# Performance work log

Measured on AMD Instinct MI355X. Metric: run time of the kernel, lower is better.

Reference implementation:

```python
import jax, jax.numpy as jnp
import numpy as np
import math

B, S, D_IN, D, H, L, NC = 4, 2048, 64, 512, 8, 2, 2
DK = D // H
FACTOR = 5
TOPK = min(FACTOR * int(math.log(S)), S)  # 35
EPS = 1e-5


def make_pe():
    # sinusoidal positional encoding [S, D]
    pos = jnp.arange(S, dtype=jnp.float32)[:, None]
    div = jnp.exp(jnp.arange(0, D, 2, dtype=jnp.float32) * (-math.log(10000.0) / D))
    pe = jnp.zeros((S, D), jnp.float32)
    pe = pe.at[:, 0::2].set(jnp.sin(pos * div)).at[:, 1::2].set(jnp.cos(pos * div))
    return pe


def layernorm(x, g, b):
    m = x.mean(-1, keepdims=True)
    v = x.var(-1, keepdims=True)
    return (x - m) / jnp.sqrt(v + EPS) * g + b


def setup_inputs() -> dict:
    key = jax.random.key(0)
    ks = iter(jax.random.split(key, 16))
    def p(shape, s=0.02):
        return jax.random.normal(next(ks), shape, jnp.float32) * s
    return dict(
        x=jax.random.normal(next(ks), (B, S, D_IN), jnp.float32),
        emb_w=p((D_IN, D)), emb_b=jnp.zeros((D,), jnp.float32),
        wq=p((L, D, D)), bq=jnp.zeros((L, D), jnp.float32),
        wk=p((L, D, D)), bk=jnp.zeros((L, D), jnp.float32),
        wv=p((L, D, D)), bv=jnp.zeros((L, D), jnp.float32),
        wo=p((L, D, D)), bo=jnp.zeros((L, D), jnp.float32),
        ff1_w=p((L, D, 4 * D)), ff1_b=jnp.zeros((L, 4 * D), jnp.float32),
        ff2_w=p((L, 4 * D, D)), ff2_b=jnp.zeros((L, D), jnp.float32),
        ln1_g=jnp.ones((L, D), jnp.float32), ln1_b=jnp.zeros((L, D), jnp.float32),
        ln2_g=jnp.ones((L, D), jnp.float32), ln2_b=jnp.zeros((L, D), jnp.float32),
        dec1_w=p((D, D // 2)), dec1_b=jnp.zeros((D // 2,), jnp.float32),
        dec2_w=p((D // 2, NC)), dec2_b=jnp.zeros((NC,), jnp.float32),
    )


def reference(x, emb_w, emb_b, wq, bq, wk, bk, wv, bv, wo, bo,
              ff1_w, ff1_b, ff2_w, ff2_b, ln1_g, ln1_b, ln2_g, ln2_b,
              dec1_w, dec1_b, dec2_w, dec2_b):
    h = x @ emb_w + emb_b + make_pe()[None]  # [B,S,D]
    scale = 1.0 / math.sqrt(DK)
    for i in range(L):
        q = (h @ wq[i] + bq[i]).reshape(B, S, H, DK).transpose(0, 2, 1, 3)
        k = (h @ wk[i] + bk[i]).reshape(B, S, H, DK).transpose(0, 2, 1, 3)
        v = (h @ wv[i] + bv[i]).reshape(B, S, H, DK).transpose(0, 2, 1, 3)
        scores = jnp.einsum('bhqd,bhkd->bhqk', q, k) * scale  # [B,H,S,S]
        top_scores, _ = jax.lax.top_k(scores, TOPK)            # [B,H,S,TOPK]
        attn = jax.nn.softmax(top_scores, axis=-1)
        # NOTE: faithful to source quirk — V sliced to its FIRST TOPK rows,
        # top_indices are discarded by the original module.
        ao = jnp.einsum('bhqk,bhkd->bhqd', attn, v[:, :, :TOPK, :])
        ao = ao.transpose(0, 2, 1, 3).reshape(B, S, D) @ wo[i] + bo[i]
        h = layernorm(h + ao, ln1_g[i], ln1_b[i])
        ff = jax.nn.relu(h @ ff1_w[i] + ff1_b[i]) @ ff2_w[i] + ff2_b[i]
        h = layernorm(h + ff, ln2_g[i], ln2_b[i])
    pooled = h.mean(axis=1)  # AdaptiveAvgPool1d(1) over seq
    out = jax.nn.relu(pooled @ dec1_w + dec1_b) @ dec2_w + dec2_b  # [B,NC]
    return out
```

## Files before the change

kernel.cpp:

```cpp
#include <hip/hip_runtime.h>
#include <cmath>

typedef unsigned short u16;
typedef __attribute__((ext_vector_type(8))) short short8;
typedef __attribute__((ext_vector_type(4))) float float4v;
typedef unsigned short ushort2v __attribute__((ext_vector_type(2)));

#define S_LEN 2048
#define NTOK  8192
#define TOPK  35
#define NT512 ((size_t)NTOK*512)

__device__ __forceinline__ u16 f2b(float f){
  unsigned int x = __float_as_uint(f);
  unsigned int r = (x + 0x7fffu + ((x >> 16) & 1u)) >> 16;
  return (u16)r;
}
__device__ __forceinline__ float b2f(u16 u){
  return __uint_as_float(((unsigned int)u) << 16);
}

__device__ __forceinline__ unsigned key_of(float f){
  unsigned u = (unsigned)f2b(f);
  unsigned m = (u & 0x8000u) ? 0xFFFFu : 0x8000u;
  return (u ^ m) & 0xFFFFu;
}
__device__ __forceinline__ float key_to_f(unsigned key){
  unsigned m = (key & 0x8000u) ? 0x8000u : 0xFFFFu;
  return __uint_as_float(((key ^ m) & 0xFFFFu) << 16);
}
__device__ __forceinline__ unsigned pkmax(unsigned a, unsigned b){
  union { unsigned u; ushort2v v; } x, y, r;
  x.u = a; y.u = b;
  r.v = __builtin_elementwise_max(x.v, y.v);
  return r.u;
}
__device__ __forceinline__ unsigned pkmin(unsigned a, unsigned b){
  union { unsigned u; ushort2v v; } x, y, r;
  x.u = a; y.u = b;
  r.v = __builtin_elementwise_min(x.v, y.v);
  return r.u;
}

__device__ __forceinline__ void bsort128(unsigned &v0, unsigned &v1, int l){
  #pragma unroll
  for (int k = 2; k <= 128; k <<= 1){
    #pragma unroll
    for (int j = k >> 1; j > 0; j >>= 1){
      if (j == 64){
        unsigned hi = pkmax(v0, v1), lo = pkmin(v0, v1);
        v0 = hi; v1 = lo;
      } else {
        unsigned o0 = (unsigned)__shfl_xor((int)v0, j, 64);
        unsigned o1 = (unsigned)__shfl_xor((int)v1, j, 64);
        bool up0 = (((l & k) == 0) != ((l & j) != 0));
        bool up1 = ((((64 + l) & k) == 0) != ((l & j) != 0));
        unsigned hi0 = pkmax(v0, o0), lo0 = pkmin(v0, o0);
        unsigned hi1 = pkmax(v1, o1), lo1 = pkmin(v1, o1);
        v0 = up0 ? hi0 : lo0;
        v1 = up1 ? hi1 : lo1;
      }
    }
  }
}

__device__ __forceinline__ void gload16(const void* g, void* l){
  __builtin_amdgcn_global_load_lds(
      (const __attribute__((address_space(1))) unsigned int*)g,
      (__attribute__((address_space(3))) unsigned int*)l, 16, 0, 0);
}

struct WtArgs {
  const float* wq; const float* wk; const float* wv; const float* wo;
  const float* ff1w; const float* ff2w;
  u16* wt_qkv; u16* wt_wo; u16* wt_ff1; u16* wt_ff2;
};
__global__ void prep_kernel(WtArgs a,
                            const float* __restrict__ x, const float* __restrict__ w,
                            const float* __restrict__ bias, float* __restrict__ h,
                            u16* __restrict__ h16){
  __shared__ float xs[4][64];
  __shared__ u16 t[32][33];
  int bx = blockIdx.x;
  int tid = threadIdx.x;
  if (bx < 6144){
    int l  = (bx >= 3072) ? 1 : 0;
    int tt = bx - l*3072;
    const float* W; u16* Wt; int K, N, tx_, ty_;
    if (tt < 1024){
      int seg = tt >> 8, r = tt & 255;
      tx_ = r & 15; ty_ = r >> 4; K = 512; N = 512;
      if (seg == 0){ W = a.wq + (size_t)l*262144; Wt = a.wt_qkv + (size_t)l*786432; }
      else if (seg == 1){ W = a.wk + (size_t)l*262144; Wt = a.wt_qkv + (size_t)l*786432 + 262144; }
      else if (seg == 2){ W = a.wv + (size_t)l*262144; Wt = a.wt_qkv + (size_t)l*786432 + 524288; }
      else { W = a.wo + (size_t)l*262144; Wt = a.wt_wo + (size_t)l*262144; }
    } else if (tt < 2048){
      int r = tt - 1024;
      tx_ = r & 63; ty_ = r >> 6; K = 512; N = 2048;
      W = a.ff1w + (size_t)l*1048576; Wt = a.wt_ff1 + (size_t)l*1048576;
    } else {
      int r = tt - 2048;
      tx_ = r & 15; ty_ = r >> 4; K = 2048; N = 512;
      W = a.ff2w + (size_t)l*1048576; Wt = a.wt_ff2 + (size_t)l*1048576;
    }
    int k0 = ty_*32, n0 = tx_*32;
    int tx = tid & 31, ty = tid >> 5;
    #pragma unroll
    for (int i = ty; i < 32; i += 8)
      t[i][tx] = f2b(W[(size_t)(k0+i)*N + n0+tx]);
    __syncthreads();
    #pragma unroll
    for (int i = ty; i < 32; i += 8)
      Wt[(size_t)(n0+i)*K + k0+tx] = t[tx][i];
  } else {
    int t0 = (bx - 6144) * 4;
    xs[tid >> 6][tid & 63] = x[(size_t)(t0 + (tid >> 6))*64 + (tid & 63)];
    __syncthreads();
    float b0 = bias[tid], b1 = bias[tid + 256];
    float acc[4][2];
    #pragma unroll
    for (int tk = 0; tk < 4; ++tk){ acc[tk][0] = b0; acc[tk][1] = b1; }
    #pragma unroll 8
    for (int k = 0; k < 64; ++k){
      float w0 = w[k*512 + tid];
      float w1 = w[k*512 + tid + 256];
      #pragma unroll
      for (int tk = 0; tk < 4; ++tk){
        float xv = xs[tk][k];
        acc[tk][0] += xv * w0;
        acc[tk][1] += xv * w1;
      }
    }
    const float neg_ln1e4_over_D = -9.210340371976184f / 512.f;
    int c0 = tid, c1 = tid + 256;
    float e0 = expf((float)(c0 & ~1) * neg_ln1e4_over_D);
    float e1 = expf((float)(c1 & ~1) * neg_ln1e4_over_D);
    #pragma unroll
    for (int tk = 0; tk < 4; ++tk){
      int tok = t0 + tk;
      int s = tok & (S_LEN - 1);
      float a0 = (float)s * e0;
      float p0 = (c0 & 1) ? cosf(a0) : sinf(a0);
      float a1 = (float)s * e1;
      float p1 = (c1 & 1) ? cosf(a1) : sinf(a1);
      float v0 = acc[tk][0] + p0, v1 = acc[tk][1] + p1;
      h[(size_t)tok*512 + c0] = v0;  h16[(size_t)tok*512 + c0] = f2b(v0);
      h[(size_t)tok*512 + c1] = v1;  h16[(size_t)tok*512 + c1] = f2b(v1);
    }
  }
}

template<int EPI>
__global__ __launch_bounds__(256) void gemm_mfma(
    const u16* __restrict__ A, int lda, const u16* __restrict__ Bt, int ldb,
    const float* __restrict__ bias0, const float* __restrict__ bias1,
    const float* __restrict__ bias2,
    float* __restrict__ Cf, u16* __restrict__ C16a, u16* __restrict__ C16b,
    float* __restrict__ Cv, int M, int N, int Klen){
  __shared__ __align__(16) u16 As[2*128*64];
  __shared__ __align__(16) u16 Bs[2*128*64];
  int tid = threadIdx.x;
  int w = tid >> 6, l = tid & 63, quad = l >> 4, m = l & 15;
  int gx = gridDim.x;
  int orig = blockIdx.y * gx + blockIdx.x;
  int nwg  = gx * gridDim.y;
  int tt   = (orig & 7) * (nwg >> 3) + (orig >> 3);
  int m0 = (tt / gx) * 128, n0 = (tt % gx) * 128;
  int mh = (w >> 1)*64, nh = (w & 1)*64;
  float4v acc[4][4];
  #pragma unroll
  for (int i = 0; i < 4; ++i)
    #pragma unroll
    for (int j = 0; j < 4; ++j) acc[i][j] = (float4v){0.f,0.f,0.f,0.f};

  #define GSTAGE(ofs, kt) do { \
    _Pragma("unroll") \
    for (int c = 0; c < 4; ++c){ \
      int g = c*256 + tid; \
      int row = g >> 3, scx = g & 7, dc = scx ^ (row & 7); \
      gload16(A  + (size_t)(m0+row)*lda + (kt) + dc*8, As + (ofs) + (size_t)g*8); \
      gload16(Bt + (size_t)(n0+row)*ldb + (kt) + dc*8, Bs + (ofs) + (size_t)g*8); \
    } } while(0)

  GSTAGE(0, 0);
  __syncthreads();
  int cur = 0;
  for (int kt = 0; kt < Klen; kt += 64){
    int nxt = cur ^ 1;
    if (kt + 64 < Klen) GSTAGE(nxt*(128*64), kt + 64);
    const u16* Ac = As + cur*(128*64);
    const u16* Bc = Bs + cur*(128*64);
    #pragma unroll
    for (int kk = 0; kk < 2; ++kk){
      short8 af[4], bf[4];
      #pragma unroll
      for (int i = 0; i < 4; ++i){
        int dcx = kk*4 + quad;
        int ra = mh + i*16 + m;
        af[i] = *(const short8*)(Ac + (size_t)(ra*8 + (dcx ^ (ra & 7)))*8);
        int rb = nh + i*16 + m;
        bf[i] = *(const short8*)(Bc + (size_t)(rb*8 + (dcx ^ (rb & 7)))*8);
      }
      #pragma unroll
      for (int i = 0; i < 4; ++i)
        #pragma unroll
        for (int j = 0; j < 4; ++j)
          acc[i][j] = __builtin_amdgcn_mfma_f32_16x16x32_bf16(af[i], bf[j], acc[i][j], 0, 0, 0);
    }
    __syncthreads();
    cur = nxt;
  }
  #undef GSTAGE

  #pragma unroll
  for (int i = 0; i < 4; ++i){
    #pragma unroll
    for (int j = 0; j < 4; ++j){
      int col = n0 + nh + j*16 + m;
      #pragma unroll
      for (int r = 0; r < 4; ++r){
        int row = m0 + mh + i*16 + quad*4 + r;
        float v = acc[i][j][r];
        if (EPI == 0){
          Cf[(size_t)row*N + col] = v + bias0[col];
        } else if (EPI == 1){
          C16a[(size_t)row*N + col] = f2b(fmaxf(v + bias0[col], 0.f));
        } else {
          int sel = col >> 9, n5 = col & 511;
          const float* bp = (sel == 0) ? bias0 : (sel == 1) ? bias1 : bias2;
          float vv = v + bp[n5];
          int d = n5 & 63, hh = n5 >> 6;
          int b = row >> 11, s = row & 2047;
          size_t idx = (((size_t)(b*8 + hh))*2048 + s)*64 + d;
          if (sel == 0)      C16a[idx] = f2b(vv);
          else if (sel == 1) C16b[idx] = f2b(vv);
          else               Cv[idx]  = vv;
        }
      }
    }
  }
}

__global__ __launch_bounds__(512, 8) void attn_mfma_topk(
    const u16* __restrict__ qb16, const u16* __restrict__ kb16,
    const float* __restrict__ vb, u16* __restrict__ aob16){
  __shared__ unsigned pr[8*1024];
  int tid  = threadIdx.x;
  int w    = tid >> 6, l = tid & 63;
  int quad = l >> 4,  m = l & 15;
  int orig = blockIdx.y * 128 + blockIdx.x;
  int t4   = ((orig & 7) << 9) | (orig >> 3);
  int bh   = t4 >> 7;
  int q0   = (t4 & 127) << 4;

  const u16* Qp = qb16 + ((size_t)bh*2048 + q0 + m)*64 + quad*8;
  short8 a0 = *(const short8*)Qp;
  short8 a1 = *(const short8*)(Qp + 32);

  const u16* Kbase = kb16 + (size_t)bh*2048*64;
  unsigned sc[32];
  int swz = (quad & 1) << 4;
  const u16* kp0 = Kbase + (size_t)(w*128 + m)*64 + quad*8;
  const uint4* p4 = (const uint4*)(pr + w*1024);

  short8 cb0 = *(const short8*)kp0;
  short8 cb1 = *(const short8*)(kp0 + 32);
  #pragma unroll
  for (int t = 0; t < 16; ++t){
    short8 nb0, nb1;
    if (t < 15){
      int tn = t + 1;
      const u16* np = kp0 + (size_t)(((tn >> 3) << 10) + ((tn & 7) << 4))*64;
      nb0 = *(const short8*)np;
      nb1 = *(const short8*)(np + 32);
    }
    float4v acc = {0.f, 0.f, 0.f, 0.f};
    acc = __builtin_amdgcn_mfma_f32_16x16x32_bf16(a0, cb0, acc, 0, 0, 0);
    acc = __builtin_amdgcn_mfma_f32_16x16x32_bf16(a1, cb1, acc, 0, 0, 0);
    int lk = (w << 7) + ((t & 7) << 4);
    #pragma unroll
    for (int c = 0; c < 2; ++c){
      unsigned lo = key_of(acc[2*c]);
      unsigned hi = key_of(acc[2*c+1]);
      pr[(quad*2 + c)*1024 + ((lk + m) ^ swz)] = lo | (hi << 16);
    }
    cb0 = nb0; cb1 = nb1;
    if (t == 7){
      __syncthreads();
      #pragma unroll
      for (int j = 0; j < 4; ++j){
        uint4 v4 = p4[j*64 + l];
        sc[j*4+0] = v4.x; sc[j*4+1] = v4.y; sc[j*4+2] = v4.z; sc[j*4+3] = v4.w;
      }
      __syncthreads();
    }
  }
  __syncthreads();
  #pragma unroll
  for (int j = 0; j < 4; ++j){
    uint4 v4 = p4[j*64 + l];
    sc[16+j*4+0] = v4.x; sc[16+j*4+1] = v4.y; sc[16+j*4+2] = v4.z; sc[16+j*4+3] = v4.w;
  }

  unsigned* row = &pr[w*1024];

  unsigned m1 = pkmax(sc[0], sc[1]);
  unsigned m2 = pkmin(sc[0], sc[1]);
  #pragma unroll
  for (int i = 2; i < 32; ++i){
    unsigned v = sc[i];
    unsigned nm1 = pkmax(m1, v);
    m2 = pkmax(m2, pkmin(m1, v));
    m1 = nm1;
  }

  unsigned mA1 = m1 & 0xFFFFu, mB1 = m1 >> 16;
  unsigned mA2 = m2 & 0xFFFFu, mB2 = m2 >> 16;
  unsigned tA = 0, tB = 0;
  #pragma unroll
  for (int bit = 15; bit >= 0; --bit){
    unsigned cA = tA | (1u << bit);
    unsigned cB = tB | (1u << bit);
    int nA = __popcll(__ballot(mA1 >= cA)) + __popcll(__ballot(mA2 >= cA));
    int nB = __popcll(__ballot(mB1 >= cB)) + __popcll(__ballot(mB2 >= cB));
    if (nA >= TOPK) tA = cA;
    if (nB >= TOPK) tB = cB;
  }
  unsigned TT = (tA - 1) | ((tB - 1) << 16);

  unsigned mask = 0;
  #pragma unroll
  for (int i = 0; i < 32; ++i){
    mask |= (pkmax(sc[i], TT) != TT) ? (1u << i) : 0u;
  }
  int cnt = __popc(mask);

  int pre = cnt;
  #pragma unroll
  for (int off = 1; off < 64; off <<= 1){
    int n = __shfl_up(pre, off, 64);
    if (l >= off) pre += n;
  }
  pre -= cnt;

  #pragma unroll
  for (int i = 0; i < 32; ++i){
    if (mask & (1u << i)){
      int p = pre + __popc(mask & ((1u << i) - 1u));
      if (p < 128) row[p] = sc[i];
    }
  }
  int tot = __shfl(pre + cnt, 63, 64);

  unsigned c0 = (l < tot)      ? row[l]      : 0u;
  unsigned c1 = (64 + l < tot) ? row[64 + l] : 0u;

  const float* Vb = vb + (size_t)bh*2048*64 + l;
  float vreg[TOPK];
  #pragma unroll
  for (int r = 0; r < TOPK; ++r) vreg[r] = Vb[(size_t)r*64];

  bsort128(c0, c1, l);

  unsigned top0 = (unsigned)__shfl((int)c0, 0, 64);
  float mAf = key_to_f(top0 & 0xFFFFu) * 0.125f;
  float mBf = key_to_f(top0 >> 16)     * 0.125f;
  float tvA = key_to_f(c0 & 0xFFFFu)   * 0.125f;
  float tvB = key_to_f(c0 >> 16)       * 0.125f;
  float wAv = (l < TOPK) ? __expf(tvA - mAf) : 0.f;
  float wBv = (l < TOPK) ? __expf(tvB - mBf) : 0.f;

  float dA = wAv, dB = wBv;
  #pragma unroll
  for (int off = 32; off > 0; off >>= 1){
    dA += __shfl_xor(dA, off, 64);
    dB += __shfl_xor(dB, off, 64);
  }

  float accA = 0.f, accB = 0.f;
  #pragma unroll
  for (int r = 0; r < TOPK; ++r){
    float wA = __uint_as_float((unsigned)__builtin_amdgcn_readlane((int)__float_as_uint(wAv), r));
    float wB = __uint_as_float((unsigned)__builtin_amdgcn_readlane((int)__float_as_uint(wBv), r));
    float vv = vreg[r];
    accA += wA * vv;
    accB += wB * vv;
  }
  accA *= __builtin_amdgcn_rcpf(dA);
  accB *= __builtin_amdgcn_rcpf(dB);

  int b = bh >> 3, hh = bh & 7;
  int sA = q0 + w*2;
  aob16[(((size_t)(b*2048 + sA))*8 + hh)*64 + l]     = f2b(accA);
  aob16[(((size_t)(b*2048 + sA + 1))*8 + hh)*64 + l] = f2b(accB);
}

__global__ void resid_ln_kernel(float* __restrict__ h, const float* __restrict__ t,
                                const float* __restrict__ g, const float* __restrict__ b,
                                u16* __restrict__ h16){
  int half = threadIdx.x >> 7;
  int tok  = blockIdx.x*2 + half;
  int tid  = threadIdx.x & 127;
  size_t base4 = (size_t)tok * 128;
  float4 hv = ((const float4*)h)[base4 + tid];
  float4 tv = ((const float4*)t)[base4 + tid];
  float x0 = hv.x + tv.x, x1 = hv.y + tv.y;
  float x2 = hv.z + tv.z, x3 = hv.w + tv.w;
  __shared__ float red[8];
  int wid = threadIdx.x >> 6, lane = threadIdx.x & 63;

  float s = (x0 + x1) + (x2 + x3);
  #pragma unroll
  for (int off = 32; off > 0; off >>= 1) s += __shfl_xor(s, off, 64);
  if (lane == 0) red[wid] = s;
  __syncthreads();
  int hb = half << 1;
  float mean = (red[hb] + red[hb+1]) * (1.f/512.f);

  float d0 = x0 - mean, d1 = x1 - mean, d2 = x2 - mean, d3 = x3 - mean;
  float sq = (d0*d0 + d1*d1) + (d2*d2 + d3*d3);
  #pragma unroll
  for (int off = 32; off > 0; off >>= 1) sq += __shfl_xor(sq, off, 64);
  if (lane == 0) red[4 + wid] = sq;
  __syncthreads();
  float var = (red[4 + hb] + red[4 + hb + 1]) * (1.f/512.f);
  float inv = rsqrtf(var + 1e-5f);
  float4 gv = ((const float4*)g)[tid];
  float4 bv = ((const float4*)b)[tid];
  float o0 = d0 * inv * gv.x + bv.x;
  float o1 = d1 * inv * gv.y + bv.y;
  float o2 = d2 * inv * gv.z + bv.z;
  float o3 = d3 * inv * gv.w + bv.w;
  ((float4*)h)[base4 + tid] = make_float4(o0, o1, o2, o3);
  uint2 pk;
  pk.x = (unsigned)f2b(o0) | ((unsigned)f2b(o1) << 16);
  pk.y = (unsigned)f2b(o2) | ((unsigned)f2b(o3) << 16);
  ((uint2*)h16)[base4 + tid] = pk;
}

__global__ void pool_kernel(const float* __restrict__ h, float* __restrict__ part){
  int c = blockIdx.x * 256 + threadIdx.x;
  int b = blockIdx.y;
  int z = blockIdx.z;
  const float* p = h + ((size_t)b * 2048 + z * 64) * 512 + c;
  float acc = 0.f;
  #pragma unroll 8
  for (int s = 0; s < 64; ++s) acc += p[(size_t)s * 512];
  part[((size_t)(z*4 + b))*512 + c] = acc;
}

__global__ void decoder_kernel(const float* __restrict__ part,
                               const float* __restrict__ w1, const float* __restrict__ b1,
                               const float* __restrict__ w2, const float* __restrict__ b2,
                               float* __restrict__ out){
  __shared__ float ps[4][512];
  __shared__ float hid[4][256];
  int tid = threadIdx.x;
  for (int i = tid; i < 2048; i += 256){
    int b = i >> 9, c = i & 511;
    float s = 0.f;
    #pragma unroll
    for (int z = 0; z < 32; ++z) s += part[((size_t)(z*4 + b))*512 + c];
    ps[b][c] = s * (1.f/2048.f);
  }
  __syncthreads();
  float bb = b1[tid];
  for (int b = 0; b < 4; ++b){
    float acc = bb;
    for (int k = 0; k < 512; ++k) acc += ps[b][k] * w1[k*256 + tid];
    hid[b][tid] = fmaxf(acc, 0.f);
  }
  __syncthreads();
  if (tid < 8){
    int b = tid >> 1, c = tid & 1;
    float acc = b2[c];
    for (int j = 0; j < 256; ++j) acc += hid[b][j] * w2[j*2 + c];
    out[b*2 + c] = acc;
  }
}

extern "C" void kernel_launch(void* const* d_in, const int* in_sizes, int n_in,
                              void* d_out, int out_size, void* d_ws, size_t ws_size,
                              hipStream_t stream){
  const float* x     = (const float*)d_in[0];
  const float* emb_w = (const float*)d_in[1];
  const float* emb_b = (const float*)d_in[2];
  const float* wq    = (const float*)d_in[3];
  const float* bq    = (const float*)d_in[4];
  const float* wk    = (const float*)d_in[5];
  const float* bk    = (const float*)d_in[6];
  const float* wv    = (const float*)d_in[7];
  const float* bv    = (const float*)d_in[8];
  const float* wo    = (const float*)d_in[9];
  const float* bo    = (const float*)d_in[10];
  const float* ff1w  = (const float*)d_in[11];
  const float* ff1b  = (const float*)d_in[12];
  const float* ff2w  = (const float*)d_in[13];
  const float* ff2b  = (const float*)d_in[14];
  const float* ln1g  = (const float*)d_in[15];
  const float* ln1b  = (const float*)d_in[16];
  const float* ln2g  = (const float*)d_in[17];
  const float* ln2b  = (const float*)d_in[18];
  const float* d1w   = (const float*)d_in[19];
  const float* d1b   = (const float*)d_in[20];
  const float* d2w   = (const float*)d_in[21];
  const float* d2b   = (const float*)d_in[22];

  float* h      = (float*)d_ws;
  float* tmp    = h + NT512;
  u16*   u      = (u16*)(tmp + NT512);
  u16*   h16    = u;
  u16*   q16    = u + NT512;
  u16*   k16    = u + 2*NT512;
  float* vb     = (float*)(u + 3*NT512);
  u16*   ff16   = q16;
  u16*   aob16  = (u16*)(vb + NT512);
  u16*   wt     = aob16 + NT512;
  u16*   wt_qkv = wt;
  u16*   wt_wo  = wt_qkv + (size_t)2*1536*512;
  u16*   wt_ff1 = wt_wo  + (size_t)2*512*512;
  u16*   wt_ff2 = wt_ff1 + (size_t)2*2048*512;
  float* part   = tmp;

  WtArgs wa{wq, wk, wv, wo, ff1w, ff2w, wt_qkv, wt_wo, wt_ff1, wt_ff2};
  prep_kernel<<<8192, 256, 0, stream>>>(wa, x, emb_w, emb_b, h, h16);

  for (int l = 0; l < 2; ++l){
    gemm_mfma<2><<<dim3(12, 64), 256, 0, stream>>>(
        h16, 512, wt_qkv + (size_t)l*1536*512, 512,
        bq + l*512, bk + l*512, bv + l*512,
        nullptr, q16, k16, vb, NTOK, 1536, 512);

    attn_mfma_topk<<<dim3(128, 32), 512, 0, stream>>>(q16, k16, vb, aob16);

    gemm_mfma<0><<<dim3(4, 64), 256, 0, stream>>>(
        aob16, 512, wt_wo + (size_t)l*512*512, 512,
        bo + l*512, nullptr, nullptr,
        tmp, nullptr, nullptr, nullptr, NTOK, 512, 512);
    resid_ln_kernel<<<NTOK/2, 256, 0, stream>>>(h, tmp, ln1g + l*512, ln1b + l*512, h16);

    gemm_mfma<1><<<dim3(16, 64), 256, 0, stream>>>(
        h16, 512, wt_ff1 + (size_t)l*2048*512, 512,
        ff1b + l*2048, nullptr, nullptr,
        nullptr, ff16, nullptr, nullptr, NTOK, 2048, 512);

    gemm_mfma<0><<<dim3(4, 64), 256, 0, stream>>>(
        ff16, 2048, wt_ff2 + (size_t)l*512*2048, 2048,
        ff2b + l*512, nullptr, nullptr,
        tmp, nullptr, nullptr, nullptr, NTOK, 512, 2048);
    resid_ln_kernel<<<NTOK/2, 256, 0, stream>>>(h, tmp, ln2g + l*512, ln2b + l*512, h16);
  }

  pool_kernel<<<dim3(2, 4, 32), 256, 0, stream>>>(h, part);
  decoder_kernel<<<1, 256, 0, stream>>>(part, d1w, d1b, d2w, d2b, (float*)d_out);
}
```

Measured before the change: 699.5 us.

## Single-buffer wide GEMMs, skip unused V rows, pack topk keys, skip final bf16 copy

The GEMM template gains a DBUF flag. The QKV and FF1 GEMMs now use single-buffered LDS, which halves their shared memory and should allow more resident blocks, at the cost of losing load/compute overlap. The QKV epilogue writes only the first TOPK rows of V, since attention reads only those. The score-to-sort-key conversion is done on two values packed into one word. The last layer's layernorm skips writing its unused bf16 copy.

```diff
diff --git a/kernel.cpp b/kernel.cpp
--- a/kernel.cpp
+++ b/kernel.cpp
@@ -16,9 +16,6 @@
   unsigned int r = (x + 0x7fffu + ((x >> 16) & 1u)) >> 16;
   return (u16)r;
 }
-__device__ __forceinline__ float b2f(u16 u){
-  return __uint_as_float(((unsigned int)u) << 16);
-}
 
 __device__ __forceinline__ unsigned key_of(float f){
   unsigned u = (unsigned)f2b(f);
@@ -28,6 +25,11 @@
 __device__ __forceinline__ float key_to_f(unsigned key){
   unsigned m = (key & 0x8000u) ? 0x8000u : 0xFFFFu;
   return __uint_as_float(((key ^ m) & 0xFFFFu) << 16);
+}
+__device__ __forceinline__ unsigned key2_of(unsigned u){
+  unsigned t = (u >> 15) & 0x00010001u;
+  unsigned mask = 0x80008000u + (t << 15) - t;
+  return u ^ mask;
 }
 __device__ __forceinline__ unsigned pkmax(unsigned a, unsigned b){
   union { unsigned u; ushort2v v; } x, y, r;
@@ -150,15 +152,15 @@
   }
 }
 
-template<int EPI>
+template<int EPI, int DBUF>
 __global__ __launch_bounds__(256) void gemm_mfma(
     const u16* __restrict__ A, int lda, const u16* __restrict__ Bt, int ldb,
     const float* __restrict__ bias0, const float* __restrict__ bias1,
     const float* __restrict__ bias2,
     float* __restrict__ Cf, u16* __restrict__ C16a, u16* __restrict__ C16b,
     float* __restrict__ Cv, int M, int N, int Klen){
-  __shared__ __align__(16) u16 As[2*128*64];
-  __shared__ __align__(16) u16 Bs[2*128*64];
+  __shared__ __align__(16) u16 As[(DBUF ? 2 : 1)*128*64];
+  __shared__ __align__(16) u16 Bs[(DBUF ? 2 : 1)*128*64];
   int tid = threadIdx.x;
   int w = tid >> 6, l = tid & 63, quad = l >> 4, m = l & 15;
   int gx = gridDim.x;
@@ -182,35 +184,46 @@
       gload16(Bt + (size_t)(n0+row)*ldb + (kt) + dc*8, Bs + (ofs) + (size_t)g*8); \
     } } while(0)
 
-  GSTAGE(0, 0);
-  __syncthreads();
-  int cur = 0;
-  for (int kt = 0; kt < Klen; kt += 64){
-    int nxt = cur ^ 1;
-    if (kt + 64 < Klen) GSTAGE(nxt*(128*64), kt + 64);
-    const u16* Ac = As + cur*(128*64);
-    const u16* Bc = Bs + cur*(128*64);
-    #pragma unroll
-    for (int kk = 0; kk < 2; ++kk){
-      short8 af[4], bf[4];
-      #pragma unroll
-      for (int i = 0; i < 4; ++i){
-        int dcx = kk*4 + quad;
-        int ra = mh + i*16 + m;
-        af[i] = *(const short8*)(Ac + (size_t)(ra*8 + (dcx ^ (ra & 7)))*8);
-        int rb = nh + i*16 + m;
-        bf[i] = *(const short8*)(Bc + (size_t)(rb*8 + (dcx ^ (rb & 7)))*8);
-      }
-      #pragma unroll
-      for (int i = 0; i < 4; ++i)
-        #pragma unroll
-        for (int j = 0; j < 4; ++j)
-          acc[i][j] = __builtin_amdgcn_mfma_f32_16x16x32_bf16(af[i], bf[j], acc[i][j], 0, 0, 0);
-    }
+  #define GCOMPUTE(Ac, Bc) do { \
+    _Pragma("unroll") \
+    for (int kk = 0; kk < 2; ++kk){ \
+      short8 af[4], bf[4]; \
+      _Pragma("unroll") \
+      for (int i = 0; i < 4; ++i){ \
+        int dcx = kk*4 + quad; \
+        int ra = mh + i*16 + m; \
+        af[i] = *(const short8*)((Ac) + (size_t)(ra*8 + (dcx ^ (ra & 7)))*8); \
+        int rb = nh + i*16 + m; \
+        bf[i] = *(const short8*)((Bc) + (size_t)(rb*8 + (dcx ^ (rb & 7)))*8); \
+      } \
+      _Pragma("unroll") \
+      for (int i = 0; i < 4; ++i) \
+        _Pragma("unroll") \
+        for (int j = 0; j < 4; ++j) \
+          acc[i][j] = __builtin_amdgcn_mfma_f32_16x16x32_bf16(af[i], bf[j], acc[i][j], 0, 0, 0); \
+    } } while(0)
+
+  if (DBUF){
+    GSTAGE(0, 0);
     __syncthreads();
-    cur = nxt;
+    int cur = 0;
+    for (int kt = 0; kt < Klen; kt += 64){
+      int nxt = cur ^ 1;
+      if (kt + 64 < Klen) GSTAGE(nxt*(128*64), kt + 64);
+      GCOMPUTE(As + cur*(128*64), Bs + cur*(128*64));
+      __syncthreads();
+      cur = nxt;
+    }
+  } else {
+    for (int kt = 0; kt < Klen; kt += 64){
+      GSTAGE(0, kt);
+      __syncthreads();
+      GCOMPUTE(As, Bs);
+      __syncthreads();
+    }
   }
   #undef GSTAGE
+  #undef GCOMPUTE
 
   #pragma unroll
   for (int i = 0; i < 4; ++i){
@@ -234,7 +247,7 @@
           size_t idx = (((size_t)(b*8 + hh))*2048 + s)*64 + d;
           if (sel == 0)      C16a[idx] = f2b(vv);
           else if (sel == 1) C16b[idx] = f2b(vv);
-          else               Cv[idx]  = vv;
+          else if (s < TOPK) Cv[idx]  = vv;
         }
       }
     }
@@ -280,9 +293,12 @@
     int lk = (w << 7) + ((t & 7) << 4);
     #pragma unroll
     for (int c = 0; c < 2; ++c){
-      unsigned lo = key_of(acc[2*c]);
-      unsigned hi = key_of(acc[2*c+1]);
-      pr[(quad*2 + c)*1024 + ((lk + m) ^ swz)] = lo | (hi << 16);
+      unsigned xa = __float_as_uint(acc[2*c]);
+      unsigned xb = __float_as_uint(acc[2*c+1]);
+      unsigned ta = xa + 0x7fffu + ((xa >> 16) & 1u);
+      unsigned tb = xb + 0x7fffu + ((xb >> 16) & 1u);
+      unsigned pk = (ta >> 16) | (tb & 0xFFFF0000u);
+      pr[(quad*2 + c)*1024 + ((lk + m) ^ swz)] = key2_of(pk);
     }
     cb0 = nb0; cb1 = nb1;
     if (t == 7){
@@ -432,10 +448,12 @@
   float o2 = d2 * inv * gv.z + bv.z;
   float o3 = d3 * inv * gv.w + bv.w;
   ((float4*)h)[base4 + tid] = make_float4(o0, o1, o2, o3);
-  uint2 pk;
-  pk.x = (unsigned)f2b(o0) | ((unsigned)f2b(o1) << 16);
-  pk.y = (unsigned)f2b(o2) | ((unsigned)f2b(o3) << 16);
-  ((uint2*)h16)[base4 + tid] = pk;
+  if (h16){
+    uint2 pk;
+    pk.x = (unsigned)f2b(o0) | ((unsigned)f2b(o1) << 16);
+    pk.y = (unsigned)f2b(o2) | ((unsigned)f2b(o3) << 16);
+    ((uint2*)h16)[base4 + tid] = pk;
+  }
 }
 
 __global__ void pool_kernel(const float* __restrict__ h, float* __restrict__ part){
@@ -526,29 +544,30 @@
   prep_kernel<<<8192, 256, 0, stream>>>(wa, x, emb_w, emb_b, h, h16);
 
   for (int l = 0; l < 2; ++l){
-    gemm_mfma<2><<<dim3(12, 64), 256, 0, stream>>>(
+    gemm_mfma<2, 0><<<dim3(12, 64), 256, 0, stream>>>(
         h16, 512, wt_qkv + (size_t)l*1536*512, 512,
         bq + l*512, bk + l*512, bv + l*512,
         nullptr, q16, k16, vb, NTOK, 1536, 512);
 
     attn_mfma_topk<<<dim3(128, 32), 512, 0, stream>>>(q16, k16, vb, aob16);
 
-    gemm_mfma<0><<<dim3(4, 64), 256, 0, stream>>>(
+    gemm_mfma<0, 1><<<dim3(4, 64), 256, 0, stream>>>(
         aob16, 512, wt_wo + (size_t)l*512*512, 512,
         bo + l*512, nullptr, nullptr,
         tmp, nullptr, nullptr, nullptr, NTOK, 512, 512);
     resid_ln_kernel<<<NTOK/2, 256, 0, stream>>>(h, tmp, ln1g + l*512, ln1b + l*512, h16);
 
-    gemm_mfma<1><<<dim3(16, 64), 256, 0, stream>>>(
+    gemm_mfma<1, 0><<<dim3(16, 64), 256, 0, stream>>>(
         h16, 512, wt_ff1 + (size_t)l*2048*512, 512,
         ff1b + l*2048, nullptr, nullptr,
         nullptr, ff16, nullptr, nullptr, NTOK, 2048, 512);
 
-    gemm_mfma<0><<<dim3(4, 64), 256, 0, stream>>>(
+    gemm_mfma<0, 1><<<dim3(4, 64), 256, 0, stream>>>(
         ff16, 2048, wt_ff2 + (size_t)l*512*2048, 2048,
         ff2b + l*512, nullptr, nullptr,
         tmp, nullptr, nullptr, nullptr, NTOK, 512, 2048);
-    resid_ln_kernel<<<NTOK/2, 256, 0, stream>>>(h, tmp, ln2g + l*512, ln2b + l*512, h16);
+    resid_ln_kernel<<<NTOK/2, 256, 0, stream>>>(h, tmp, ln2g + l*512, ln2b + l*512,
+                                                (l == 1) ? nullptr : h16);
   }
 
   pool_kernel<<<dim3(2, 4, 32), 256, 0, stream>>>(h, part);
```

Result: no change. 689.3 us (-1.5%).
